# Optimization experiments

Hardware: AMD Instinct MI355X
Metric: run time of the kernel (lower is better)

The kernel has to match this reference:

```python
import jax, jax.numpy as jnp
import numpy as np

N = 4096
F_IN = 3
T_DIM = 3
H_DIM = 128
N_HEADS = 4
HEAD_DIM = H_DIM // N_HEADS
OUT_DIM = 128
LN_EPS = 1e-5


def _layernorm(x, g, b):
    mu = jnp.mean(x, axis=-1, keepdims=True)
    var = jnp.mean(jnp.square(x - mu), axis=-1, keepdims=True)
    return (x - mu) * jax.lax.rsqrt(var + LN_EPS) * g + b


def setup_inputs() -> dict:
    key = jax.random.key(0)
    ks = jax.random.split(key, 16)
    enriched = F_IN + T_DIM
    d = {}
    d["node_features"] = jax.random.uniform(ks[0], (N, F_IN), dtype=jnp.float32)
    d["adj_matrix"] = jax.random.uniform(ks[1], (N, N), dtype=jnp.float32)
    d["trigger_context"] = jax.random.uniform(ks[2], (T_DIM,), dtype=jnp.float32)
    # node_projection: Linear(enriched, H_DIM) + LayerNorm
    d["Wp"] = jax.random.normal(ks[3], (H_DIM, enriched), dtype=jnp.float32) * 0.3
    d["bp"] = jnp.zeros((H_DIM,), jnp.float32)
    d["ln1_g"] = jnp.ones((H_DIM,), jnp.float32)
    d["ln1_b"] = jnp.zeros((H_DIM,), jnp.float32)
    # Q/K/V projections (no bias)
    d["Wq"] = jax.random.normal(ks[4], (H_DIM, H_DIM), dtype=jnp.float32) * 0.08
    d["Wk"] = jax.random.normal(ks[5], (H_DIM, H_DIM), dtype=jnp.float32) * 0.08
    d["Wv"] = jax.random.normal(ks[6], (H_DIM, H_DIM), dtype=jnp.float32) * 0.08
    # trigger_temperature: Linear(T_DIM, H_DIM//2) -> ReLU -> Linear(H_DIM//2, N_HEADS) -> Softplus
    d["Wt1"] = jax.random.normal(ks[7], (H_DIM // 2, T_DIM), dtype=jnp.float32) * 0.5
    d["bt1"] = jnp.zeros((H_DIM // 2,), jnp.float32)
    d["Wt2"] = jax.random.normal(ks[8], (N_HEADS, H_DIM // 2), dtype=jnp.float32) * 0.15
    d["bt2"] = jnp.zeros((N_HEADS,), jnp.float32)
    # trigger_gate: Linear(T_DIM, H_DIM) -> Sigmoid
    d["Wg"] = jax.random.normal(ks[9], (H_DIM, T_DIM), dtype=jnp.float32) * 0.5
    d["bg"] = jnp.zeros((H_DIM,), jnp.float32)
    d["stb"] = jnp.zeros((N_HEADS,), jnp.float32)  # stateful_trigger_bias
    # output_projection: Linear(H_DIM, OUT_DIM) + LayerNorm
    d["Wo"] = jax.random.normal(ks[10], (OUT_DIM, H_DIM), dtype=jnp.float32) * 0.08
    d["bo"] = jnp.zeros((OUT_DIM,), jnp.float32)
    d["ln2_g"] = jnp.ones((OUT_DIM,), jnp.float32)
    d["ln2_b"] = jnp.zeros((OUT_DIM,), jnp.float32)
    d["res_scale"] = jnp.ones((1,), jnp.float32) * 0.1
    return d


def reference(node_features, adj_matrix, trigger_context, Wp, bp, ln1_g, ln1_b,
              Wq, Wk, Wv, Wt1, bt1, Wt2, bt2, Wg, bg, stb, Wo, bo,
              ln2_g, ln2_b, res_scale):
    n = node_features.shape[0]
    # 1. Enrichment: concat trigger context to every node
    trig_b = jnp.broadcast_to(trigger_context[None, :], (n, T_DIM))
    enriched = jnp.concatenate([node_features, trig_b], axis=1)  # [N, 6]
    # 2. Projection: Linear -> LayerNorm -> ReLU (dropout identity in eval)
    h = jax.nn.relu(_layernorm(enriched @ Wp.T + bp, ln1_g, ln1_b))  # [N, H_DIM]
    # 3. Multi-head Q/K/V
    Q = (h @ Wq.T).reshape(n, N_HEADS, HEAD_DIM)
    K = (h @ Wk.T).reshape(n, N_HEADS, HEAD_DIM)
    V = (h @ Wv.T).reshape(n, N_HEADS, HEAD_DIM)
    scores = jnp.einsum('ihd,jhd->ijh', Q, K) / jnp.sqrt(jnp.float32(HEAD_DIM))  # [N,N,H]
    # trigger-conditioned temperature per head
    temp = jax.nn.softplus(jax.nn.relu(trigger_context @ Wt1.T + bt1) @ Wt2.T + bt2)
    temp = jnp.clip(temp, 0.1, 5.0)  # [H]
    scores = scores / temp[None, None, :]
    # adjacency mask
    scores = jnp.where((adj_matrix == 0.0)[:, :, None], jnp.float32(-1e9), scores)
    # stateful x trigger interaction bias
    is_reactive = 1.0 - trigger_context[0]
    is_stateful = node_features[:, 2]
    stateful_matrix = jnp.outer(is_stateful, is_stateful)  # [N,N]
    scores = scores + stateful_matrix[:, :, None] * (stb * is_reactive)[None, None, :]
    # softmax over neighbors (dim j)
    attn = jax.nn.softmax(scores, axis=1)  # [N,N,H]
    # trigger gate (scalar mean of sigmoid gate)
    gate_value = jnp.mean(jax.nn.sigmoid(trigger_context @ Wg.T + bg))
    attn = attn * gate_value
    # aggregation
    agg = jnp.einsum('ijh,jhd->ihd', attn, V).reshape(n, H_DIM)
    out = _layernorm(agg @ Wo.T + bo, ln2_g, ln2_b) + res_scale * h[:, :OUT_DIM]
    return out
```

## Files before the change

kernel.cpp:

```cpp
#include <hip/hip_runtime.h>


#define NNODES 4096
#define BI     32
#define JSPLIT 4
#define JCHUNK (NNODES / JSPLIT)
#define NT     (JCHUNK / 32)

typedef float    f32x4 __attribute__((ext_vector_type(4)));
typedef _Float16 f16x8 __attribute__((ext_vector_type(8)));
typedef __fp16   fp16x2 __attribute__((ext_vector_type(2)));

#define P_PARAMS 0
#define P_STF    256
#define P_H      4352
#define P_QH     528640
#define P_KH     790784
#define P_VT     1052928
#define P_PAGG   1315072
#define P_PML    3412224
#define PP_SCALE 0
#define PP_STB2  4
#define PP_GATE  8
#define PP_CTRIG 16

__device__ __forceinline__ unsigned pk_f16(float lo, float hi) {
  union { fp16x2 h; unsigned u; } c;
  c.h = __builtin_amdgcn_cvt_pkrtz(lo, hi);
  return c.u;
}

__global__ __launch_bounds__(128) void k1_trigger(
    const float* __restrict__ trig,
    const float* __restrict__ Wp, const float* __restrict__ bp,
    const float* __restrict__ Wt1, const float* __restrict__ bt1,
    const float* __restrict__ Wt2, const float* __restrict__ bt2,
    const float* __restrict__ Wg, const float* __restrict__ bg,
    const float* __restrict__ stb,
    float* __restrict__ ws)
{
  __shared__ float s_t1[64];
  __shared__ float s_red[2];
  const int t = threadIdx.x;
  const float t0 = trig[0], t1v = trig[1], t2 = trig[2];

  ws[P_PARAMS + PP_CTRIG + t] = bp[t] + t0 * Wp[t*6+3] + t1v * Wp[t*6+4] + t2 * Wp[t*6+5];

  if (t < 64) {
    float a = bt1[t] + t0 * Wt1[t*3+0] + t1v * Wt1[t*3+1] + t2 * Wt1[t*3+2];
    s_t1[t] = fmaxf(a, 0.f);
  }
  float gx = bg[t] + t0 * Wg[t*3+0] + t1v * Wg[t*3+1] + t2 * Wg[t*3+2];
  float gs = 1.f / (1.f + __expf(-gx));
  for (int off = 1; off < 64; off <<= 1) gs += __shfl_xor(gs, off);
  if ((t & 63) == 0) s_red[t >> 6] = gs;
  __syncthreads();
  if (t == 0) ws[P_PARAMS + PP_GATE] = (s_red[0] + s_red[1]) * (1.f / 128.f);
  if (t < 4) {
    float acc = bt2[t];
    for (int k = 0; k < 64; ++k) acc += Wt2[t*64+k] * s_t1[k];
    float sp = (acc > 20.f) ? acc : log1pf(__expf(acc));
    float temp = fminf(fmaxf(sp, 0.1f), 5.f);
    const float LOG2E = 1.4426950408889634f;
    ws[P_PARAMS + PP_SCALE + t] = LOG2E / (5.656854249492380f * temp);
    ws[P_PARAMS + PP_STB2  + t] = stb[t] * (1.f - t0) * LOG2E;
  }
}

__global__ __launch_bounds__(128) void k2_h(
    const float* __restrict__ nf, const float* __restrict__ Wp,
    const float* __restrict__ g, const float* __restrict__ b,
    float* __restrict__ ws)
{
  const int i = blockIdx.x, j = threadIdx.x;
  const float* ctrig = ws + P_PARAMS + PP_CTRIG;
  const float n0 = nf[i*3+0], n1 = nf[i*3+1], n2 = nf[i*3+2];
  const float x = ctrig[j] + n0 * Wp[j*6+0] + n1 * Wp[j*6+1] + n2 * Wp[j*6+2];
  float s = x, sq = x * x;
  for (int off = 1; off < 64; off <<= 1) { s += __shfl_xor(s, off); sq += __shfl_xor(sq, off); }
  __shared__ float red[2][2];
  if ((j & 63) == 0) { red[j >> 6][0] = s; red[j >> 6][1] = sq; }
  __syncthreads();
  const float mu = (red[0][0] + red[1][0]) * (1.f / 128.f);
  const float var = (red[0][1] + red[1][1]) * (1.f / 128.f) - mu * mu;
  const float rs = rsqrtf(var + 1e-5f);
  const float hv = fmaxf((x - mu) * rs * g[j] + b[j], 0.f);
  ws[P_H + (size_t)i * 128 + j] = hv;
  if (j == 0) ws[P_STF + i] = n2;
}

__global__ __launch_bounds__(256) void k3_qkv(
    const float* __restrict__ Wq, const float* __restrict__ Wk,
    const float* __restrict__ Wv, float* __restrict__ ws)
{
  __shared__ float h_s[32][129];
  __shared__ float w_s[32][128];
  __shared__ float o_s[32][132];
  const int t = threadIdx.x;
  const int r0 = blockIdx.x * 32;
  const int mat = blockIdx.y;
  const float* W = (mat == 0) ? Wq : (mat == 1) ? Wk : Wv;
  const float* hp = ws + P_H;

  {
    const int r = t >> 3, kb = (t & 7) << 4;
    const float4* src = (const float4*)(hp + (size_t)(r0 + r) * 128 + kb);
#pragma unroll
    for (int p = 0; p < 4; ++p) {
      float4 v = src[p];
      h_s[r][kb + 4*p + 0] = v.x; h_s[r][kb + 4*p + 1] = v.y;
      h_s[r][kb + 4*p + 2] = v.z; h_s[r][kb + 4*p + 3] = v.w;
    }
  }

  const int rr = t & 31, cs = (t >> 5) << 4;
  float acc[16];
#pragma unroll
  for (int e = 0; e < 16; ++e) acc[e] = 0.f;

  for (int kc = 0; kc < 4; ++kc) {
    __syncthreads();
    {
      const int c = t >> 1, kk = (t & 1) << 4;
      const float4* srcw = (const float4*)(W + c * 128 + kc * 32 + kk);
#pragma unroll
      for (int p = 0; p < 4; ++p) {
        float4 v = srcw[p];
        w_s[kk + 4*p + 0][c] = v.x; w_s[kk + 4*p + 1][c] = v.y;
        w_s[kk + 4*p + 2][c] = v.z; w_s[kk + 4*p + 3][c] = v.w;
      }
    }
    __syncthreads();
#pragma unroll
    for (int k = 0; k < 32; ++k) {
      const float a = h_s[rr][kc * 32 + k];
      const float4 w0 = *(const float4*)&w_s[k][cs + 0];
      const float4 w1 = *(const float4*)&w_s[k][cs + 4];
      const float4 w2 = *(const float4*)&w_s[k][cs + 8];
      const float4 w3 = *(const float4*)&w_s[k][cs + 12];
      acc[0]  += a * w0.x; acc[1]  += a * w0.y; acc[2]  += a * w0.z; acc[3]  += a * w0.w;
      acc[4]  += a * w1.x; acc[5]  += a * w1.y; acc[6]  += a * w1.z; acc[7]  += a * w1.w;
      acc[8]  += a * w2.x; acc[9]  += a * w2.y; acc[10] += a * w2.z; acc[11] += a * w2.w;
      acc[12] += a * w3.x; acc[13] += a * w3.y; acc[14] += a * w3.z; acc[15] += a * w3.w;
    }
  }

  const float* params = ws + P_PARAMS;
  if (mat < 2) {
    unsigned short* dst = (unsigned short*)(ws + (mat == 0 ? P_QH : P_KH));
    const float sc = (mat == 0) ? params[PP_SCALE + (cs >> 5)] : 1.f;
    uint4 w0, w1;
    w0.x = pk_f16(acc[0]*sc,  acc[1]*sc);  w0.y = pk_f16(acc[2]*sc,  acc[3]*sc);
    w0.z = pk_f16(acc[4]*sc,  acc[5]*sc);  w0.w = pk_f16(acc[6]*sc,  acc[7]*sc);
    w1.x = pk_f16(acc[8]*sc,  acc[9]*sc);  w1.y = pk_f16(acc[10]*sc, acc[11]*sc);
    w1.z = pk_f16(acc[12]*sc, acc[13]*sc); w1.w = pk_f16(acc[14]*sc, acc[15]*sc);
    *(uint4*)(dst + (size_t)(r0 + rr) * 128 + cs)     = w0;
    *(uint4*)(dst + (size_t)(r0 + rr) * 128 + cs + 8) = w1;
  } else {
#pragma unroll
    for (int e = 0; e < 16; ++e) o_s[rr][cs + e] = acc[e];
    __syncthreads();
    unsigned short* vt = (unsigned short*)(ws + P_VT);
    const int c = t >> 1, rb = (t & 1) << 4;
    float v[16];
#pragma unroll
    for (int mm = 0; mm < 16; ++mm) v[mm] = o_s[rb + mm][c];
    uint4 w0, w1;
    w0.x = pk_f16(v[0],  v[1]);  w0.y = pk_f16(v[2],  v[3]);
    w0.z = pk_f16(v[4],  v[5]);  w0.w = pk_f16(v[6],  v[7]);
    w1.x = pk_f16(v[8],  v[9]);  w1.y = pk_f16(v[10], v[11]);
    w1.z = pk_f16(v[12], v[13]); w1.w = pk_f16(v[14], v[15]);
    *(uint4*)(vt + (size_t)c * 4096 + r0 + rb)     = w0;
    *(uint4*)(vt + (size_t)c * 4096 + r0 + rb + 8) = w1;
  }
}

__global__ __launch_bounds__(256) void k4_attn(
    const float* __restrict__ adj, float* __restrict__ ws)
{
  __shared__ float adj_s[2][BI][36];
  const int tid = threadIdx.x;
  const int w = tid >> 6, l = tid & 63, li = l & 15, g = l >> 4;
  const int i0 = blockIdx.x * BI;
  const int jbeg = blockIdx.y * JCHUNK;
  const _Float16* Qh = (const _Float16*)(ws + P_QH);
  const _Float16* Kh = (const _Float16*)(ws + P_KH);
  const _Float16* VT = (const _Float16*)(ws + P_VT);
  const float* stf = ws + P_STF;
  const float* params = ws + P_PARAMS;

  f16x8 qf[2];
  float a_stb[2], m[2], lsum[2];
  f32x4 agg[2][2];
#pragma unroll
  for (int it = 0; it < 2; ++it) {
    qf[it] = *(const f16x8*)(Qh + (size_t)(i0 + it*16 + li) * 128 + w * 32 + g * 8);
    a_stb[it] = stf[i0 + it*16 + li] * params[PP_STB2 + w];
    m[it] = -1e30f; lsum[it] = 0.f;
    agg[it][0] = (f32x4){0.f, 0.f, 0.f, 0.f};
    agg[it][1] = (f32x4){0.f, 0.f, 0.f, 0.f};
  }

  const int sr = tid >> 3, sjb = (tid & 7) << 2;
  const float* adj_base = adj + (size_t)(i0 + sr) * 4096 + jbeg + sjb;
  f32x4 reg = __builtin_nontemporal_load((const f32x4*)adj_base);
  *(f32x4*)&adj_s[0][sr][sjb] = reg;

  for (int t = 0; t < NT; ++t) {
    if (t + 1 < NT)
      reg = __builtin_nontemporal_load((const f32x4*)(adj_base + (t + 1) * 32));
    __syncthreads();
    const int buf = t & 1;
    const int jt = jbeg + t * 32;

    const f16x8 kf0 = *(const f16x8*)(Kh + (size_t)(jt + li) * 128 + w * 32 + g * 8);
    const f16x8 kf1 = *(const f16x8*)(Kh + (size_t)(jt + 16 + li) * 128 + w * 32 + g * 8);

    union { unsigned u[4]; f16x8 h; } vf0, vf1;
    {
      const _Float16* vr0 = VT + (size_t)(w * 32 + li) * 4096 + jt + g * 4;
      uint2 va = *(const uint2*)vr0;
      uint2 vb = *(const uint2*)(vr0 + 16);
      vf0.u[0] = va.x; vf0.u[1] = va.y; vf0.u[2] = vb.x; vf0.u[3] = vb.y;
      const _Float16* vr1 = vr0 + 16 * 4096;
      uint2 vc = *(const uint2*)vr1;
      uint2 vd = *(const uint2*)(vr1 + 16);
      vf1.u[0] = vc.x; vf1.u[1] = vc.y; vf1.u[2] = vd.x; vf1.u[3] = vd.y;
    }

    const f32x4 st0 = *(const f32x4*)(stf + jt + g * 4);
    const f32x4 st1 = *(const f32x4*)(stf + jt + 16 + g * 4);

#pragma unroll
    for (int it = 0; it < 2; ++it) {
      const f32x4 zero = {0.f, 0.f, 0.f, 0.f};
      f32x4 c0 = __builtin_amdgcn_mfma_f32_16x16x32_f16(kf0, qf[it], zero, 0, 0, 0);
      f32x4 c1 = __builtin_amdgcn_mfma_f32_16x16x32_f16(kf1, qf[it], zero, 0, 0, 0);

      const f32x4 ad0 = *(const f32x4*)&adj_s[buf][it*16 + li][g * 4];
      const f32x4 ad1 = *(const f32x4*)&adj_s[buf][it*16 + li][16 + g * 4];

      float s0[4], s1[4];
#pragma unroll
      for (int e = 0; e < 4; ++e) {
        s0[e] = ((ad0[e] == 0.f) ? -1e9f : c0[e]) + a_stb[it] * st0[e];
        s1[e] = ((ad1[e] == 0.f) ? -1e9f : c1[e]) + a_stb[it] * st1[e];
      }

      float mx = fmaxf(fmaxf(fmaxf(s0[0], s0[1]), fmaxf(s0[2], s0[3])),
                       fmaxf(fmaxf(s1[0], s1[1]), fmaxf(s1[2], s1[3])));
      mx = fmaxf(mx, __shfl_xor(mx, 16));
      mx = fmaxf(mx, __shfl_xor(mx, 32));
      const float mn = fmaxf(m[it], mx);
      const float f = exp2f(m[it] - mn);
      float p0[4], p1[4];
#pragma unroll
      for (int e = 0; e < 4; ++e) { p0[e] = exp2f(s0[e] - mn); p1[e] = exp2f(s1[e] - mn); }
      float ts = ((p0[0] + p0[1]) + (p0[2] + p0[3])) + ((p1[0] + p1[1]) + (p1[2] + p1[3]));
      ts += __shfl_xor(ts, 16);
      ts += __shfl_xor(ts, 32);
      lsum[it] = lsum[it] * f + ts;
      m[it] = mn;
#pragma unroll
      for (int e = 0; e < 4; ++e) { agg[it][0][e] *= f; agg[it][1][e] *= f; }

      union { unsigned u[4]; f16x8 h; } pb;
      pb.u[0] = pk_f16(p0[0], p0[1]);
      pb.u[1] = pk_f16(p0[2], p0[3]);
      pb.u[2] = pk_f16(p1[0], p1[1]);
      pb.u[3] = pk_f16(p1[2], p1[3]);

      agg[it][0] = __builtin_amdgcn_mfma_f32_16x16x32_f16(vf0.h, pb.h, agg[it][0], 0, 0, 0);
      agg[it][1] = __builtin_amdgcn_mfma_f32_16x16x32_f16(vf1.h, pb.h, agg[it][1], 0, 0, 0);
    }

    if (t + 1 < NT)
      *(f32x4*)&adj_s[(t + 1) & 1][sr][sjb] = reg;
  }

#pragma unroll
  for (int it = 0; it < 2; ++it) {
    float* pagg = ws + P_PAGG + ((size_t)(blockIdx.y * 4 + w) * 4096 + (i0 + it*16 + li)) * 32;
    *(f32x4*)(pagg + g * 4)      = agg[it][0];
    *(f32x4*)(pagg + 16 + g * 4) = agg[it][1];
    if (g == 0) {
      float* pml = ws + P_PML + ((size_t)(blockIdx.y * 4 + w) * 4096 + (i0 + it*16 + li)) * 2;
      pml[0] = m[it];
      pml[1] = lsum[it];
    }
  }
}

__global__ __launch_bounds__(256) void k5_out(
    const float* __restrict__ Wo, const float* __restrict__ bo,
    const float* __restrict__ g2, const float* __restrict__ b2,
    const float* __restrict__ res_scale,
    float* __restrict__ ws, float* __restrict__ out)
{
  __shared__ float wo_s[64][128];
  __shared__ float agg_s[16][132];
  __shared__ float red[16][16][2];
  __shared__ float mu_s[16], rs_s[16];
  const int t = threadIdx.x;
  const int i0 = blockIdx.x * 16;

  {
    const float gate = ws[P_PARAMS + PP_GATE];
    const int hd = t & 127, ih = t >> 7;
    const int h = hd >> 5, d = hd & 31;
    for (int ir = 0; ir < 8; ++ir) {
      const int il = ih * 8 + ir;
      const int i = i0 + il;
      float mv[JSPLIT], lv[JSPLIT];
      float mm = -1e30f;
#pragma unroll
      for (int sp = 0; sp < JSPLIT; ++sp) {
        const float* ml = ws + P_PML + ((size_t)(sp * 4 + h) * 4096 + i) * 2;
        mv[sp] = ml[0]; lv[sp] = ml[1];
        mm = fmaxf(mm, mv[sp]);
      }
      float lt = 0.f, av = 0.f;
#pragma unroll
      for (int sp = 0; sp < JSPLIT; ++sp) {
        const float wgt = exp2f(mv[sp] - mm);
        lt += lv[sp] * wgt;
        av += ws[P_PAGG + ((size_t)(sp * 4 + h) * 4096 + i) * 32 + d] * wgt;
      }
      agg_s[il][hd] = av * gate / lt;
    }
  }

  const int r = t & 15, cs = (t >> 4) << 3;
  float acc[8];
#pragma unroll
  for (int e = 0; e < 8; ++e) acc[e] = bo[cs + e];

  for (int kh = 0; kh < 2; ++kh) {
    __syncthreads();
    {
      const int c = t >> 1, kb = (t & 1) << 5;
      const float4* src = (const float4*)(Wo + c * 128 + kh * 64 + kb);
#pragma unroll
      for (int q = 0; q < 8; ++q) {
        float4 v = src[q];
        wo_s[kb + 4*q + 0][c] = v.x; wo_s[kb + 4*q + 1][c] = v.y;
        wo_s[kb + 4*q + 2][c] = v.z; wo_s[kb + 4*q + 3][c] = v.w;
      }
    }
    __syncthreads();
    for (int k = 0; k < 64; ++k) {
      const float a = agg_s[r][kh * 64 + k];
      const float4 w0 = *(const float4*)&wo_s[k][cs];
      const float4 w1 = *(const float4*)&wo_s[k][cs + 4];
      acc[0] += a * w0.x; acc[1] += a * w0.y; acc[2] += a * w0.z; acc[3] += a * w0.w;
      acc[4] += a * w1.x; acc[5] += a * w1.y; acc[6] += a * w1.z; acc[7] += a * w1.w;
    }
  }

  float s = 0.f, sq = 0.f;
#pragma unroll
  for (int e = 0; e < 8; ++e) { s += acc[e]; sq += acc[e] * acc[e]; }
  red[r][t >> 4][0] = s; red[r][t >> 4][1] = sq;
  __syncthreads();
  if (t < 16) {
    float ss = 0.f, qq = 0.f;
    for (int q = 0; q < 16; ++q) { ss += red[t][q][0]; qq += red[t][q][1]; }
    const float mu = ss * (1.f / 128.f);
    const float var = qq * (1.f / 128.f) - mu * mu;
    mu_s[t] = mu; rs_s[t] = rsqrtf(var + 1e-5f);
  }
  __syncthreads();
  const float mu = mu_s[r], rs = rs_s[r];
  const float rsc = res_scale[0];
  const float* hrow = ws + P_H + (size_t)(i0 + r) * 128 + cs;
  const float4 h0 = *(const float4*)(hrow), h1 = *(const float4*)(hrow + 4);
  const float4 ga = *(const float4*)(g2 + cs), gb = *(const float4*)(g2 + cs + 4);
  const float4 ba = *(const float4*)(b2 + cs), bb = *(const float4*)(b2 + cs + 4);
  float4 o0, o1;
  o0.x = (acc[0] - mu) * rs * ga.x + ba.x + rsc * h0.x;
  o0.y = (acc[1] - mu) * rs * ga.y + ba.y + rsc * h0.y;
  o0.z = (acc[2] - mu) * rs * ga.z + ba.z + rsc * h0.z;
  o0.w = (acc[3] - mu) * rs * ga.w + ba.w + rsc * h0.w;
  o1.x = (acc[4] - mu) * rs * gb.x + bb.x + rsc * h1.x;
  o1.y = (acc[5] - mu) * rs * gb.y + bb.y + rsc * h1.y;
  o1.z = (acc[6] - mu) * rs * gb.z + bb.z + rsc * h1.z;
  o1.w = (acc[7] - mu) * rs * gb.w + bb.w + rsc * h1.w;
  *(float4*)(out + (size_t)(i0 + r) * 128 + cs)     = o0;
  *(float4*)(out + (size_t)(i0 + r) * 128 + cs + 4) = o1;
}

extern "C" void kernel_launch(void* const* d_in, const int* in_sizes, int n_in,
                              void* d_out, int out_size, void* d_ws, size_t ws_size,
                              hipStream_t stream) {
  const float* nf   = (const float*)d_in[0];
  const float* adj  = (const float*)d_in[1];
  const float* trig = (const float*)d_in[2];
  const float* Wp   = (const float*)d_in[3];
  const float* bp   = (const float*)d_in[4];
  const float* ln1g = (const float*)d_in[5];
  const float* ln1b = (const float*)d_in[6];
  const float* Wq   = (const float*)d_in[7];
  const float* Wk   = (const float*)d_in[8];
  const float* Wv   = (const float*)d_in[9];
  const float* Wt1  = (const float*)d_in[10];
  const float* bt1  = (const float*)d_in[11];
  const float* Wt2  = (const float*)d_in[12];
  const float* bt2  = (const float*)d_in[13];
  const float* Wg   = (const float*)d_in[14];
  const float* bg   = (const float*)d_in[15];
  const float* stb  = (const float*)d_in[16];
  const float* Wo   = (const float*)d_in[17];
  const float* bo   = (const float*)d_in[18];
  const float* ln2g = (const float*)d_in[19];
  const float* ln2b = (const float*)d_in[20];
  const float* rsc  = (const float*)d_in[21];
  float* ws  = (float*)d_ws;
  float* out = (float*)d_out;

  hipLaunchKernelGGL(k1_trigger, dim3(1), dim3(128), 0, stream,
                     trig, Wp, bp, Wt1, bt1, Wt2, bt2, Wg, bg, stb, ws);
  hipLaunchKernelGGL(k2_h, dim3(NNODES), dim3(128), 0, stream, nf, Wp, ln1g, ln1b, ws);
  hipLaunchKernelGGL(k3_qkv, dim3(128, 3), dim3(256), 0, stream, Wq, Wk, Wv, ws);
  hipLaunchKernelGGL(k4_attn, dim3(NNODES / BI, JSPLIT), dim3(256), 0, stream, adj, ws);
  hipLaunchKernelGGL(k5_out, dim3(256), dim3(256), 0, stream, Wo, bo, ln2g, ln2b, rsc, ws, out);
}
```

Before: 230.8 us.

## Remove trigger kernel, prefetch K/V tiles, lazy rescale, and double JSPLIT

Removes the single-block trigger kernel and recomputes its small parameters inside the projection, QKV, attention and output kernels, cutting one launch and a serial dependency. The attention kernel now double-buffers the K, V and stateful-feature loads in registers one tile ahead. It skips the online-softmax rescale when no lane's max grows, and defers the row-sum shuffles to the end. It also doubles the j-split to 8 so more blocks run in parallel, which adds launch-bounds occupancy pressure and doubles the partial buffers that the output kernel has to merge.

```diff
diff --git a/kernel.cpp b/kernel.cpp
--- a/kernel.cpp
+++ b/kernel.cpp
@@ -3,7 +3,7 @@
 
 #define NNODES 4096
 #define BI     32
-#define JSPLIT 4
+#define JSPLIT 8
 #define JCHUNK (NNODES / JSPLIT)
 #define NT     (JCHUNK / 32)
 
@@ -11,18 +11,15 @@
 typedef _Float16 f16x8 __attribute__((ext_vector_type(8)));
 typedef __fp16   fp16x2 __attribute__((ext_vector_type(2)));
 
-#define P_PARAMS 0
 #define P_STF    256
 #define P_H      4352
 #define P_QH     528640
 #define P_KH     790784
 #define P_VT     1052928
 #define P_PAGG   1315072
-#define P_PML    3412224
-#define PP_SCALE 0
-#define PP_STB2  4
-#define PP_GATE  8
-#define PP_CTRIG 16
+#define P_PML    5509376
+
+#define LOG2E 1.4426950408889634f
 
 __device__ __forceinline__ unsigned pk_f16(float lo, float hi) {
   union { fp16x2 h; unsigned u; } c;
@@ -30,52 +27,18 @@
   return c.u;
 }
 
-__global__ __launch_bounds__(128) void k1_trigger(
-    const float* __restrict__ trig,
+__global__ __launch_bounds__(128) void k2_h(
+    const float* __restrict__ nf, const float* __restrict__ trig,
     const float* __restrict__ Wp, const float* __restrict__ bp,
-    const float* __restrict__ Wt1, const float* __restrict__ bt1,
-    const float* __restrict__ Wt2, const float* __restrict__ bt2,
-    const float* __restrict__ Wg, const float* __restrict__ bg,
-    const float* __restrict__ stb,
-    float* __restrict__ ws)
-{
-  __shared__ float s_t1[64];
-  __shared__ float s_red[2];
-  const int t = threadIdx.x;
-  const float t0 = trig[0], t1v = trig[1], t2 = trig[2];
-
-  ws[P_PARAMS + PP_CTRIG + t] = bp[t] + t0 * Wp[t*6+3] + t1v * Wp[t*6+4] + t2 * Wp[t*6+5];
-
-  if (t < 64) {
-    float a = bt1[t] + t0 * Wt1[t*3+0] + t1v * Wt1[t*3+1] + t2 * Wt1[t*3+2];
-    s_t1[t] = fmaxf(a, 0.f);
-  }
-  float gx = bg[t] + t0 * Wg[t*3+0] + t1v * Wg[t*3+1] + t2 * Wg[t*3+2];
-  float gs = 1.f / (1.f + __expf(-gx));
-  for (int off = 1; off < 64; off <<= 1) gs += __shfl_xor(gs, off);
-  if ((t & 63) == 0) s_red[t >> 6] = gs;
-  __syncthreads();
-  if (t == 0) ws[P_PARAMS + PP_GATE] = (s_red[0] + s_red[1]) * (1.f / 128.f);
-  if (t < 4) {
-    float acc = bt2[t];
-    for (int k = 0; k < 64; ++k) acc += Wt2[t*64+k] * s_t1[k];
-    float sp = (acc > 20.f) ? acc : log1pf(__expf(acc));
-    float temp = fminf(fmaxf(sp, 0.1f), 5.f);
-    const float LOG2E = 1.4426950408889634f;
-    ws[P_PARAMS + PP_SCALE + t] = LOG2E / (5.656854249492380f * temp);
-    ws[P_PARAMS + PP_STB2  + t] = stb[t] * (1.f - t0) * LOG2E;
-  }
-}
-
-__global__ __launch_bounds__(128) void k2_h(
-    const float* __restrict__ nf, const float* __restrict__ Wp,
     const float* __restrict__ g, const float* __restrict__ b,
     float* __restrict__ ws)
 {
   const int i = blockIdx.x, j = threadIdx.x;
-  const float* ctrig = ws + P_PARAMS + PP_CTRIG;
+  const float t0 = trig[0], t1v = trig[1], t2 = trig[2];
   const float n0 = nf[i*3+0], n1 = nf[i*3+1], n2 = nf[i*3+2];
-  const float x = ctrig[j] + n0 * Wp[j*6+0] + n1 * Wp[j*6+1] + n2 * Wp[j*6+2];
+  const float* wr = Wp + j * 6;
+  const float x = bp[j] + n0 * wr[0] + n1 * wr[1] + n2 * wr[2]
+                        + t0 * wr[3] + t1v * wr[4] + t2 * wr[5];
   float s = x, sq = x * x;
   for (int off = 1; off < 64; off <<= 1) { s += __shfl_xor(s, off); sq += __shfl_xor(sq, off); }
   __shared__ float red[2][2];
@@ -91,11 +54,16 @@
 
 __global__ __launch_bounds__(256) void k3_qkv(
     const float* __restrict__ Wq, const float* __restrict__ Wk,
-    const float* __restrict__ Wv, float* __restrict__ ws)
+    const float* __restrict__ Wv, const float* __restrict__ trig,
+    const float* __restrict__ Wt1, const float* __restrict__ bt1,
+    const float* __restrict__ Wt2, const float* __restrict__ bt2,
+    float* __restrict__ ws)
 {
   __shared__ float h_s[32][129];
   __shared__ float w_s[32][128];
   __shared__ float o_s[32][132];
+  __shared__ float t1_s[64];
+  __shared__ float scale_s[4];
   const int t = threadIdx.x;
   const int r0 = blockIdx.x * 32;
   const int mat = blockIdx.y;
@@ -111,6 +79,18 @@
       h_s[r][kb + 4*p + 0] = v.x; h_s[r][kb + 4*p + 1] = v.y;
       h_s[r][kb + 4*p + 2] = v.z; h_s[r][kb + 4*p + 3] = v.w;
     }
+  }
+  if (t < 64) {
+    float a = bt1[t] + trig[0] * Wt1[t*3+0] + trig[1] * Wt1[t*3+1] + trig[2] * Wt1[t*3+2];
+    t1_s[t] = fmaxf(a, 0.f);
+  }
+  __syncthreads();
+  if (t < 4) {
+    float acc = bt2[t];
+    for (int k = 0; k < 64; ++k) acc += Wt2[t*64+k] * t1_s[k];
+    float sp = (acc > 20.f) ? acc : log1pf(__expf(acc));
+    float temp = fminf(fmaxf(sp, 0.1f), 5.f);
+    scale_s[t] = LOG2E / (5.656854249492380f * temp);
   }
 
   const int rr = t & 31, cs = (t >> 5) << 4;
@@ -145,10 +125,9 @@
     }
   }
 
-  const float* params = ws + P_PARAMS;
   if (mat < 2) {
     unsigned short* dst = (unsigned short*)(ws + (mat == 0 ? P_QH : P_KH));
-    const float sc = (mat == 0) ? params[PP_SCALE + (cs >> 5)] : 1.f;
+    const float sc = (mat == 0) ? scale_s[cs >> 5] : 1.f;
     uint4 w0, w1;
     w0.x = pk_f16(acc[0]*sc,  acc[1]*sc);  w0.y = pk_f16(acc[2]*sc,  acc[3]*sc);
     w0.z = pk_f16(acc[4]*sc,  acc[5]*sc);  w0.w = pk_f16(acc[6]*sc,  acc[7]*sc);
@@ -175,8 +154,9 @@
   }
 }
 
-__global__ __launch_bounds__(256) void k4_attn(
-    const float* __restrict__ adj, float* __restrict__ ws)
+__global__ __launch_bounds__(256, 4) void k4_attn(
+    const float* __restrict__ adj, const float* __restrict__ trig,
+    const float* __restrict__ stb, float* __restrict__ ws)
 {
   __shared__ float adj_s[2][BI][36];
   const int tid = threadIdx.x;
@@ -187,106 +167,113 @@
   const _Float16* Kh = (const _Float16*)(ws + P_KH);
   const _Float16* VT = (const _Float16*)(ws + P_VT);
   const float* stf = ws + P_STF;
-  const float* params = ws + P_PARAMS;
+  const float stb_eff = stb[w] * (1.f - trig[0]) * LOG2E;
 
   f16x8 qf[2];
-  float a_stb[2], m[2], lsum[2];
+  float a_stb[2], m[2], pls[2];
   f32x4 agg[2][2];
 #pragma unroll
   for (int it = 0; it < 2; ++it) {
     qf[it] = *(const f16x8*)(Qh + (size_t)(i0 + it*16 + li) * 128 + w * 32 + g * 8);
-    a_stb[it] = stf[i0 + it*16 + li] * params[PP_STB2 + w];
-    m[it] = -1e30f; lsum[it] = 0.f;
+    a_stb[it] = stf[i0 + it*16 + li] * stb_eff;
+    m[it] = -1e30f; pls[it] = 0.f;
     agg[it][0] = (f32x4){0.f, 0.f, 0.f, 0.f};
     agg[it][1] = (f32x4){0.f, 0.f, 0.f, 0.f};
   }
 
   const int sr = tid >> 3, sjb = (tid & 7) << 2;
   const float* adj_base = adj + (size_t)(i0 + sr) * 4096 + jbeg + sjb;
-  f32x4 reg = __builtin_nontemporal_load((const f32x4*)adj_base);
-  *(f32x4*)&adj_s[0][sr][sjb] = reg;
-
-  for (int t = 0; t < NT; ++t) {
-    if (t + 1 < NT)
-      reg = __builtin_nontemporal_load((const f32x4*)(adj_base + (t + 1) * 32));
-    __syncthreads();
-    const int buf = t & 1;
-    const int jt = jbeg + t * 32;
-
-    const f16x8 kf0 = *(const f16x8*)(Kh + (size_t)(jt + li) * 128 + w * 32 + g * 8);
-    const f16x8 kf1 = *(const f16x8*)(Kh + (size_t)(jt + 16 + li) * 128 + w * 32 + g * 8);
-
+
+  f16x8 kf0A, kf1A, kf0B, kf1B;
+  uint2 vaA, vbA, vcA, vdA, vaB, vbB, vcB, vdB;
+  f32x4 st0A, st1A, st0B, st1B;
+
+#define LOADF(jtv, S) do { \
+    kf0##S = *(const f16x8*)(Kh + (size_t)((jtv) + li) * 128 + w * 32 + g * 8); \
+    kf1##S = *(const f16x8*)(Kh + (size_t)((jtv) + 16 + li) * 128 + w * 32 + g * 8); \
+    const _Float16* vr_ = VT + (size_t)(w * 32 + li) * 4096 + (jtv) + g * 4; \
+    va##S = *(const uint2*)vr_;                 vb##S = *(const uint2*)(vr_ + 16); \
+    vc##S = *(const uint2*)(vr_ + 16*4096);     vd##S = *(const uint2*)(vr_ + 16*4096 + 16); \
+    st0##S = *(const f32x4*)(stf + (jtv) + g * 4); \
+    st1##S = *(const f32x4*)(stf + (jtv) + 16 + g * 4); \
+  } while (0)
+
+  auto compute = [&](const f16x8& kf0, const f16x8& kf1,
+                     const uint2& va, const uint2& vb, const uint2& vc, const uint2& vd,
+                     const f32x4& st0, const f32x4& st1, int buf) {
     union { unsigned u[4]; f16x8 h; } vf0, vf1;
-    {
-      const _Float16* vr0 = VT + (size_t)(w * 32 + li) * 4096 + jt + g * 4;
-      uint2 va = *(const uint2*)vr0;
-      uint2 vb = *(const uint2*)(vr0 + 16);
-      vf0.u[0] = va.x; vf0.u[1] = va.y; vf0.u[2] = vb.x; vf0.u[3] = vb.y;
-      const _Float16* vr1 = vr0 + 16 * 4096;
-      uint2 vc = *(const uint2*)vr1;
-      uint2 vd = *(const uint2*)(vr1 + 16);
-      vf1.u[0] = vc.x; vf1.u[1] = vc.y; vf1.u[2] = vd.x; vf1.u[3] = vd.y;
-    }
-
-    const f32x4 st0 = *(const f32x4*)(stf + jt + g * 4);
-    const f32x4 st1 = *(const f32x4*)(stf + jt + 16 + g * 4);
-
+    vf0.u[0] = va.x; vf0.u[1] = va.y; vf0.u[2] = vb.x; vf0.u[3] = vb.y;
+    vf1.u[0] = vc.x; vf1.u[1] = vc.y; vf1.u[2] = vd.x; vf1.u[3] = vd.y;
 #pragma unroll
     for (int it = 0; it < 2; ++it) {
       const f32x4 zero = {0.f, 0.f, 0.f, 0.f};
       f32x4 c0 = __builtin_amdgcn_mfma_f32_16x16x32_f16(kf0, qf[it], zero, 0, 0, 0);
       f32x4 c1 = __builtin_amdgcn_mfma_f32_16x16x32_f16(kf1, qf[it], zero, 0, 0, 0);
-
       const f32x4 ad0 = *(const f32x4*)&adj_s[buf][it*16 + li][g * 4];
       const f32x4 ad1 = *(const f32x4*)&adj_s[buf][it*16 + li][16 + g * 4];
-
       float s0[4], s1[4];
 #pragma unroll
       for (int e = 0; e < 4; ++e) {
         s0[e] = ((ad0[e] == 0.f) ? -1e9f : c0[e]) + a_stb[it] * st0[e];
         s1[e] = ((ad1[e] == 0.f) ? -1e9f : c1[e]) + a_stb[it] * st1[e];
       }
-
-      float mx = fmaxf(fmaxf(fmaxf(s0[0], s0[1]), fmaxf(s0[2], s0[3])),
-                       fmaxf(fmaxf(s1[0], s1[1]), fmaxf(s1[2], s1[3])));
-      mx = fmaxf(mx, __shfl_xor(mx, 16));
-      mx = fmaxf(mx, __shfl_xor(mx, 32));
-      const float mn = fmaxf(m[it], mx);
-      const float f = exp2f(m[it] - mn);
+      const float pl = fmaxf(fmaxf(fmaxf(s0[0], s0[1]), fmaxf(s0[2], s0[3])),
+                             fmaxf(fmaxf(s1[0], s1[1]), fmaxf(s1[2], s1[3])));
+      if (!__all(pl <= m[it])) {
+        float mx = fmaxf(pl, __shfl_xor(pl, 16));
+        mx = fmaxf(mx, __shfl_xor(mx, 32));
+        const float mn = fmaxf(m[it], mx);
+        const float f = exp2f(m[it] - mn);
+        m[it] = mn;
+        pls[it] *= f;
+#pragma unroll
+        for (int e = 0; e < 4; ++e) { agg[it][0][e] *= f; agg[it][1][e] *= f; }
+      }
       float p0[4], p1[4];
 #pragma unroll
-      for (int e = 0; e < 4; ++e) { p0[e] = exp2f(s0[e] - mn); p1[e] = exp2f(s1[e] - mn); }
-      float ts = ((p0[0] + p0[1]) + (p0[2] + p0[3])) + ((p1[0] + p1[1]) + (p1[2] + p1[3]));
-      ts += __shfl_xor(ts, 16);
-      ts += __shfl_xor(ts, 32);
-      lsum[it] = lsum[it] * f + ts;
-      m[it] = mn;
-#pragma unroll
-      for (int e = 0; e < 4; ++e) { agg[it][0][e] *= f; agg[it][1][e] *= f; }
-
+      for (int e = 0; e < 4; ++e) { p0[e] = exp2f(s0[e] - m[it]); p1[e] = exp2f(s1[e] - m[it]); }
+      pls[it] += ((p0[0] + p0[1]) + (p0[2] + p0[3])) + ((p1[0] + p1[1]) + (p1[2] + p1[3]));
       union { unsigned u[4]; f16x8 h; } pb;
       pb.u[0] = pk_f16(p0[0], p0[1]);
       pb.u[1] = pk_f16(p0[2], p0[3]);
       pb.u[2] = pk_f16(p1[0], p1[1]);
       pb.u[3] = pk_f16(p1[2], p1[3]);
-
       agg[it][0] = __builtin_amdgcn_mfma_f32_16x16x32_f16(vf0.h, pb.h, agg[it][0], 0, 0, 0);
       agg[it][1] = __builtin_amdgcn_mfma_f32_16x16x32_f16(vf1.h, pb.h, agg[it][1], 0, 0, 0);
     }
-
-    if (t + 1 < NT)
-      *(f32x4*)&adj_s[(t + 1) & 1][sr][sjb] = reg;
-  }
+  };
+
+  f32x4 rg = __builtin_nontemporal_load((const f32x4*)adj_base);
+  *(f32x4*)&adj_s[0][sr][sjb] = rg;
+  LOADF(jbeg, A);
+
+  for (int t = 0; t < NT; t += 2) {
+    rg = __builtin_nontemporal_load((const f32x4*)(adj_base + (t + 1) * 32));
+    __syncthreads();
+    LOADF(jbeg + (t + 1) * 32, B);
+    compute(kf0A, kf1A, vaA, vbA, vcA, vdA, st0A, st1A, 0);
+    *(f32x4*)&adj_s[1][sr][sjb] = rg;
+    if (t + 2 < NT)
+      rg = __builtin_nontemporal_load((const f32x4*)(adj_base + (t + 2) * 32));
+    __syncthreads();
+    if (t + 2 < NT) LOADF(jbeg + (t + 2) * 32, A);
+    compute(kf0B, kf1B, vaB, vbB, vcB, vdB, st0B, st1B, 1);
+    if (t + 2 < NT) *(f32x4*)&adj_s[0][sr][sjb] = rg;
+  }
+#undef LOADF
 
 #pragma unroll
   for (int it = 0; it < 2; ++it) {
+    float ls = pls[it];
+    ls += __shfl_xor(ls, 16);
+    ls += __shfl_xor(ls, 32);
     float* pagg = ws + P_PAGG + ((size_t)(blockIdx.y * 4 + w) * 4096 + (i0 + it*16 + li)) * 32;
     *(f32x4*)(pagg + g * 4)      = agg[it][0];
     *(f32x4*)(pagg + 16 + g * 4) = agg[it][1];
     if (g == 0) {
       float* pml = ws + P_PML + ((size_t)(blockIdx.y * 4 + w) * 4096 + (i0 + it*16 + li)) * 2;
       pml[0] = m[it];
-      pml[1] = lsum[it];
+      pml[1] = ls;
     }
   }
 }
@@ -295,17 +282,28 @@
     const float* __restrict__ Wo, const float* __restrict__ bo,
     const float* __restrict__ g2, const float* __restrict__ b2,
     const float* __restrict__ res_scale,
+    const float* __restrict__ trig, const float* __restrict__ Wg,
+    const float* __restrict__ bg,
     float* __restrict__ ws, float* __restrict__ out)
 {
   __shared__ float wo_s[64][128];
   __shared__ float agg_s[16][132];
   __shared__ float red[16][16][2];
   __shared__ float mu_s[16], rs_s[16];
+  __shared__ float gate_red[2];
   const int t = threadIdx.x;
   const int i0 = blockIdx.x * 16;
 
+  if (t < 128) {
+    float gx = bg[t] + trig[0] * Wg[t*3+0] + trig[1] * Wg[t*3+1] + trig[2] * Wg[t*3+2];
+    float gs = 1.f / (1.f + __expf(-gx));
+    for (int off = 1; off < 64; off <<= 1) gs += __shfl_xor(gs, off);
+    if ((t & 63) == 0) gate_red[t >> 6] = gs;
+  }
+  __syncthreads();
+  const float gate = (gate_red[0] + gate_red[1]) * (1.f / 128.f);
+
   {
-    const float gate = ws[P_PARAMS + PP_GATE];
     const int hd = t & 127, ih = t >> 7;
     const int h = hd >> 5, d = hd & 31;
     for (int ir = 0; ir < 8; ++ir) {
@@ -417,10 +415,10 @@
   float* ws  = (float*)d_ws;
   float* out = (float*)d_out;
 
-  hipLaunchKernelGGL(k1_trigger, dim3(1), dim3(128), 0, stream,
-                     trig, Wp, bp, Wt1, bt1, Wt2, bt2, Wg, bg, stb, ws);
-  hipLaunchKernelGGL(k2_h, dim3(NNODES), dim3(128), 0, stream, nf, Wp, ln1g, ln1b, ws);
-  hipLaunchKernelGGL(k3_qkv, dim3(128, 3), dim3(256), 0, stream, Wq, Wk, Wv, ws);
-  hipLaunchKernelGGL(k4_attn, dim3(NNODES / BI, JSPLIT), dim3(256), 0, stream, adj, ws);
-  hipLaunchKernelGGL(k5_out, dim3(256), dim3(256), 0, stream, Wo, bo, ln2g, ln2b, rsc, ws, out);
-}
+  hipLaunchKernelGGL(k2_h, dim3(NNODES), dim3(128), 0, stream, nf, trig, Wp, bp, ln1g, ln1b, ws);
+  hipLaunchKernelGGL(k3_qkv, dim3(128, 3), dim3(256), 0, stream,
+                     Wq, Wk, Wv, trig, Wt1, bt1, Wt2, bt2, ws);
+  hipLaunchKernelGGL(k4_attn, dim3(NNODES / BI, JSPLIT), dim3(256), 0, stream, adj, trig, stb, ws);
+  hipLaunchKernelGGL(k5_out, dim3(256), dim3(256), 0, stream,
+                     Wo, bo, ln2g, ln2b, rsc, trig, Wg, bg, ws, out);
+}
```

New measurement: 228.8 us. No clear change (-0.9%).
